# Performance work log

Measured on AMD Instinct MI355X. Metric: run time of the kernel, lower is better.

## Reference

```python
import jax, jax.numpy as jnp
import numpy as np

B, T, C = 4, 2048, 1024
H = 16
D = C // H  # head_dim = 64


def setup_inputs() -> dict:
    key = jax.random.key(0)
    ks = jax.random.split(key, 5)
    scale_in = 1.0 / np.sqrt(C)
    x = jax.random.normal(ks[0], (B, T, C), dtype=jnp.float32)
    w_qkv = jax.random.normal(ks[1], (C, 3 * C), dtype=jnp.float32) * scale_in
    b_qkv = jnp.zeros((3 * C,), dtype=jnp.float32)
    w_proj = jax.random.normal(ks[2], (C, C), dtype=jnp.float32) * scale_in
    b_proj = jnp.zeros((C,), dtype=jnp.float32)
    return {"x": x, "w_qkv": w_qkv, "b_qkv": b_qkv, "w_proj": w_proj, "b_proj": b_proj}


def reference(x, w_qkv, b_qkv, w_proj, b_proj):
    # fused QKV projection: [B,T,3C]
    qkv = x @ w_qkv + b_qkv
    q, k, v = jnp.split(qkv, 3, axis=-1)
    # [B,T,C] -> [B,H,T,D]
    q = q.reshape(B, T, H, D).transpose(0, 2, 1, 3)
    k = k.reshape(B, T, H, D).transpose(0, 2, 1, 3)
    v = v.reshape(B, T, H, D).transpose(0, 2, 1, 3)
    scale = 1.0 / np.sqrt(D)
    scores = jnp.einsum('bhqd,bhkd->bhqk', q, k) * scale  # [B,H,T,T]
    causal = jnp.tril(jnp.ones((T, T), dtype=bool))
    scores = jnp.where(causal, scores, jnp.finfo(scores.dtype).min)
    attn = jax.nn.softmax(scores, axis=-1)
    y = jnp.einsum('bhqk,bhkd->bhqd', attn, v)  # [B,H,T,D]
    y = y.transpose(0, 2, 1, 3).reshape(B, T, C)
    return y @ w_proj + b_proj
```

## Files before the change

### kernel.cpp

```cpp
#include <hip/hip_runtime.h>

typedef unsigned short u16;
typedef unsigned int u32;
typedef unsigned long long u64;
typedef __attribute__((ext_vector_type(8))) short s16x8;
typedef __attribute__((ext_vector_type(4))) float f32x4;

#if __has_builtin(__builtin_amdgcn_exp2f)
#define EXP2(x) __builtin_amdgcn_exp2f(x)
#else
#define EXP2(x) __expf((x) * 0.69314718f)
#endif

#if __has_builtin(__builtin_amdgcn_rcpf)
#define RCP(x) __builtin_amdgcn_rcpf(x)
#else
#define RCP(x) (1.0f / (x))
#endif

#define GLL(gp, lp) __builtin_amdgcn_global_load_lds(                         \
    (const __attribute__((address_space(1))) unsigned int*)(const void*)(gp), \
    (__attribute__((address_space(3))) unsigned int*)(void*)(lp), 16, 0, 0)

__device__ __forceinline__ u16 f2bf(float f) {
    union { float f; u32 u; } v; v.f = f;
    u32 r = v.u + 0x7FFF + ((v.u >> 16) & 1);
    return (u16)(r >> 16);
}

__device__ __forceinline__ u32 pack2_trunc(float a, float b) {
    union { float f; u32 u; } x, y; x.f = a; y.f = b;
    return (x.u >> 16) | (y.u & 0xFFFF0000u);
}

__device__ __forceinline__ float bf2f(u16 b) {
    union { u32 u; float f; } v; v.u = ((u32)b) << 16;
    return v.f;
}

__device__ __forceinline__ s16x8 scale_frag(s16x8 v, float s) {
    s16x8 o;
#pragma unroll
    for (int i = 0; i < 8; i++) o[i] = (short)f2bf(bf2f((u16)v[i]) * s);
    return o;
}

__global__ __launch_bounds__(256) void prep_fused(const float* __restrict__ x,
                                                  u16* __restrict__ x_bf,
                                                  const float* __restrict__ w_qkv,
                                                  u16* __restrict__ wqkvT,
                                                  const float* __restrict__ w_proj,
                                                  u16* __restrict__ wprojT) {
    __shared__ float tile[32][33];
    int bid = blockIdx.x, tid = threadIdx.x;
    if (bid < 8192) {
        size_t i = ((size_t)bid * 256 + tid) * 4;
        float4 f = *(const float4*)(x + i);
        u16 o[4] = { f2bf(f.x), f2bf(f.y), f2bf(f.z), f2bf(f.w) };
        *(u64*)(x_bf + i) =
            (u64)o[0] | ((u64)o[1] << 16) | ((u64)o[2] << 32) | ((u64)o[3] << 48);
        return;
    }
    const float* in;
    u16* out;
    int cols, bx, by;
    if (bid < 8192 + 3072) {
        int l = bid - 8192;
        in = w_qkv; out = wqkvT; cols = 3072; bx = l % 96; by = l / 96;
    } else {
        int l = bid - 11264;
        in = w_proj; out = wprojT; cols = 1024; bx = l & 31; by = l >> 5;
    }
    const int rows = 1024;
    int c0 = bx * 32, r0 = by * 32;
    int tx = tid & 31, ty = tid >> 5;
    for (int i = 0; i < 32; i += 8)
        tile[ty + i][tx] = in[(size_t)(r0 + ty + i) * cols + (c0 + tx)];
    __syncthreads();
    for (int i = 0; i < 32; i += 8)
        out[(size_t)(c0 + ty + i) * rows + (r0 + tx)] = f2bf(tile[tx][ty + i]);
}

template<int MODE, int NB>
__global__ __launch_bounds__(256, 4) void gemm_bt64(const u16* __restrict__ A,
                                                    const u16* __restrict__ BT,
                                                    const float* __restrict__ bias,
                                                    void* __restrict__ O1,
                                                    u16* __restrict__ vT,
                                                    int M, int N, int K) {
    __shared__ u16 SMEM[18432];
    u16* As = SMEM;
    u16* Bs = SMEM + 8192;
    int id = blockIdx.x;
    int xcd = id & 7, s = id >> 3;
    int ni = s % NB, mi8 = s / NB;
    int n0 = ni * 128, m0 = (xcd * 8 + mi8) * 128;
    int tid = threadIdx.x, lane = tid & 63, w = tid >> 6;
    int row16 = lane & 15, quad = lane >> 4;
    int wm = (w >> 1) * 64, wn = (w & 1) * 64;
    f32x4 acc[4][4] = {};

    int lr = lane >> 3;
    int cswz = (lane & 7) ^ lr;
    const u16* Ag = A + (size_t)(m0 + w * 32 + lr) * K + cswz * 8;
    const u16* Bg = BT + (size_t)(n0 + w * 32 + lr) * K + cswz * 8;
    u16* Asl = As + (w * 32) * 64;
    u16* Bsl = Bs + (w * 32) * 64;

    for (int k0 = 0; k0 < K; k0 += 64) {
        __syncthreads();
#pragma unroll
        for (int j = 0; j < 4; j++) {
            GLL(Ag + k0 + (size_t)j * 8 * K, Asl + j * 8 * 64);
            GLL(Bg + k0 + (size_t)j * 8 * K, Bsl + j * 8 * 64);
        }
        __syncthreads();
#pragma unroll
        for (int kk = 0; kk < 2; kk++) {
            s16x8 af[4], bf[4];
#pragma unroll
            for (int mi = 0; mi < 4; mi++)
                af[mi] = *(const s16x8*)&As[(wm + mi * 16 + row16) * 64 +
                                            (((kk * 4 + quad) ^ (row16 & 7)) * 8)];
#pragma unroll
            for (int ni2 = 0; ni2 < 4; ni2++)
                bf[ni2] = *(const s16x8*)&Bs[(wn + ni2 * 16 + row16) * 64 +
                                             (((kk * 4 + quad) ^ (row16 & 7)) * 8)];
#pragma unroll
            for (int mi = 0; mi < 4; mi++)
#pragma unroll
                for (int ni2 = 0; ni2 < 4; ni2++)
                    acc[mi][ni2] = __builtin_amdgcn_mfma_f32_16x16x32_bf16(
                        af[mi], bf[ni2], acc[mi][ni2], 0, 0, 0);
        }
    }

    if (MODE == 0) {
        float* O = (float*)O1;
#pragma unroll
        for (int ni2 = 0; ni2 < 4; ni2++) {
            int col = n0 + wn + ni2 * 16 + row16;
            float bv = bias[col];
#pragma unroll
            for (int mi = 0; mi < 4; mi++)
#pragma unroll
                for (int r = 0; r < 4; r++)
                    O[(size_t)(m0 + wm + mi * 16 + quad * 4 + r) * N + col] =
                        acc[mi][ni2][r] + bv;
        }
    } else if (n0 < 2048) {
        u16* qk = (u16*)O1;
#pragma unroll
        for (int ni2 = 0; ni2 < 4; ni2++) {
            int col = n0 + wn + ni2 * 16 + row16;
            float bv = bias[col];
#pragma unroll
            for (int mi = 0; mi < 4; mi++)
#pragma unroll
                for (int r = 0; r < 4; r++)
                    qk[(size_t)(m0 + wm + mi * 16 + quad * 4 + r) * 2048 + col] =
                        f2bf(acc[mi][ni2][r] + bv);
        }
    } else {
        __syncthreads();
        u16* scr = SMEM + w * 64 * 72;
#pragma unroll
        for (int ni2 = 0; ni2 < 4; ni2++) {
            float bv = bias[n0 + wn + ni2 * 16 + row16];
#pragma unroll
            for (int mi = 0; mi < 4; mi++)
#pragma unroll
                for (int r = 0; r < 4; r++)
                    scr[(ni2 * 16 + row16) * 72 + (mi * 16 + quad * 4 + r)] =
                        f2bf(acc[mi][ni2][r] + bv);
        }
        __syncthreads();
        int r8 = lane >> 3, c8 = lane & 7;
        int vbase = (m0 >> 11) * 1024 + (n0 - 2048) + wn;
        int tb = (m0 & 2047) + wm;
#pragma unroll
        for (int it = 0; it < 8; it++) {
            s16x8 vv = *(const s16x8*)&scr[(it * 8 + r8) * 72 + c8 * 8];
            *(s16x8*)&vT[(size_t)(vbase + it * 8 + r8) * 2048 + tb + c8 * 8] = vv;
        }
    }
}

__global__ __launch_bounds__(256, 2) void attn_kernel(const u16* __restrict__ qk,
                                                      const u16* __restrict__ vT,
                                                      u16* __restrict__ y) {
    __shared__ u16 Kb[2][4096];
    __shared__ u16 Vb[2][4096];
    __shared__ u16 Ps[4][2048];

    int tid = threadIdx.x, lane = tid & 63, w = tid >> 6;
    int row16 = lane & 15, quad = lane >> 4;
    int id = blockIdx.x;
    int xcd = id & 7, slot = id >> 3;
    int qt = 15 - (slot >> 3);
    int bh = ((slot & 7) << 3) | xcd;
    int b = bh >> 4, h = bh & 15;
    const u16* qkb = qk + (size_t)b * 2048 * 2048;
    const u16* vtb = vT + ((size_t)(b * 1024) + h * 64) * 2048;

    int lr = lane >> 3, cswz = (lane & 7) ^ lr;
    const u16* Kg = qkb + (size_t)(w * 16 + lr) * 2048 + 1024 + h * 64 + cswz * 8;
    const u16* Vg = vtb + (size_t)(w * 16 + lr) * 2048 + cswz * 8;
    u16* Psw = Ps[w];
    int sw = row16 & 7;

    s16x8 ones;
#pragma unroll
    for (int i = 0; i < 8; i++) ones[i] = (short)0x3F80;
    const float qs = 0.125f * 1.44269504f;

    int q0 = qt * 128;
    int niter = 2 * qt + 2;
    int qw = q0 + w * 32;

    s16x8 qf[2][2];
#pragma unroll
    for (int mi = 0; mi < 2; mi++) {
        const u16* qp = qkb + (size_t)(qw + mi * 16 + row16) * 2048 + h * 64 + quad * 8;
        qf[mi][0] = scale_frag(*(const s16x8*)qp, qs);
        qf[mi][1] = scale_frag(*(const s16x8*)(qp + 32), qs);
    }

    f32x4 acc_o[2][4] = {};
    f32x4 acc_l[2] = {};

#pragma unroll
    for (int j = 0; j < 2; j++) {
        GLL(Kg + (size_t)j * 8 * 2048, Kb[0] + w * 16 * 64 + j * 8 * 64);
        GLL(Vg + (size_t)j * 8 * 2048, Vb[0] + w * 16 * 64 + j * 8 * 64);
    }

    for (int kb = 0; kb < niter; kb++) {
        int cur = kb & 1;
        __syncthreads();
        if (kb + 1 < niter) {
            int k1 = (kb + 1) * 64;
#pragma unroll
            for (int j = 0; j < 2; j++) {
                GLL(Kg + (size_t)(k1 + j * 8) * 2048, Kb[cur ^ 1] + w * 16 * 64 + j * 8 * 64);
                GLL(Vg + k1 + (size_t)j * 8 * 2048, Vb[cur ^ 1] + w * 16 * 64 + j * 8 * 64);
            }
        }
        int k0 = kb * 64;
        if (k0 > qw + 31) continue;
        const u16* Kc = Kb[cur];
        const u16* Vc = Vb[cur];

        f32x4 sc[2][4];
#pragma unroll
        for (int nk = 0; nk < 4; nk++) {
            s16x8 kf0 = *(const s16x8*)&Kc[(nk * 16 + row16) * 64 + ((quad ^ sw) * 8)];
            s16x8 kf1 = *(const s16x8*)&Kc[(nk * 16 + row16) * 64 + (((4 + quad) ^ sw) * 8)];
#pragma unroll
            for (int mi = 0; mi < 2; mi++) {
                f32x4 z = {};
                z = __builtin_amdgcn_mfma_f32_16x16x32_bf16(kf0, qf[mi][0], z, 0, 0, 0);
                z = __builtin_amdgcn_mfma_f32_16x16x32_bf16(kf1, qf[mi][1], z, 0, 0, 0);
                sc[mi][nk] = z;
            }
        }
        if (k0 + 63 > qw) {
#pragma unroll
            for (int mi = 0; mi < 2; mi++) {
                int qg = qw + mi * 16 + row16;
#pragma unroll
                for (int nk = 0; nk < 4; nk++) {
                    int kbase = k0 + nk * 16 + quad * 4;
#pragma unroll
                    for (int r = 0; r < 4; r++)
                        if (kbase + r > qg) sc[mi][nk][r] = -__builtin_inff();
                }
            }
        }
#pragma unroll
        for (int mi = 0; mi < 2; mi++)
#pragma unroll
            for (int nk = 0; nk < 4; nk++) {
                float p0 = EXP2(sc[mi][nk][0]);
                float p1 = EXP2(sc[mi][nk][1]);
                float p2 = EXP2(sc[mi][nk][2]);
                float p3 = EXP2(sc[mi][nk][3]);
                u32 w0 = pack2_trunc(p0, p1);
                u32 w1 = pack2_trunc(p2, p3);
                int u = nk * 2 + (quad >> 1);
                int eo = ((u ^ sw) * 8) + (quad & 1) * 4;
                *(u64*)&Psw[mi * 1024 + row16 * 64 + eo] = (u64)w0 | ((u64)w1 << 32);
            }
#pragma unroll
        for (int kk = 0; kk < 2; kk++) {
            int co = ((kk * 4 + quad) ^ sw) * 8;
            s16x8 pf0 = *(const s16x8*)&Psw[row16 * 64 + co];
            s16x8 pf1 = *(const s16x8*)&Psw[1024 + row16 * 64 + co];
#pragma unroll
            for (int nd = 0; nd < 4; nd++) {
                s16x8 vf = *(const s16x8*)&Vc[(nd * 16 + row16) * 64 + co];
                acc_o[0][nd] = __builtin_amdgcn_mfma_f32_16x16x32_bf16(pf0, vf, acc_o[0][nd], 0, 0, 0);
                acc_o[1][nd] = __builtin_amdgcn_mfma_f32_16x16x32_bf16(pf1, vf, acc_o[1][nd], 0, 0, 0);
            }
            acc_l[0] = __builtin_amdgcn_mfma_f32_16x16x32_bf16(pf0, ones, acc_l[0], 0, 0, 0);
            acc_l[1] = __builtin_amdgcn_mfma_f32_16x16x32_bf16(pf1, ones, acc_l[1], 0, 0, 0);
        }
    }

#pragma unroll
    for (int mi = 0; mi < 2; mi++) {
        int t0 = qw + mi * 16 + quad * 4;
#pragma unroll
        for (int r = 0; r < 4; r++) {
            float inv = RCP(acc_l[mi][r]);
#pragma unroll
            for (int nd = 0; nd < 4; nd++)
                y[((size_t)b * 2048 + t0 + r) * 1024 + h * 64 + nd * 16 + row16] =
                    f2bf(acc_o[mi][nd][r] * inv);
        }
    }
}

extern "C" void kernel_launch(void* const* d_in, const int* in_sizes, int n_in,
                              void* d_out, int out_size, void* d_ws, size_t ws_size,
                              hipStream_t stream) {
    const float* x      = (const float*)d_in[0];
    const float* w_qkv  = (const float*)d_in[1];
    const float* b_qkv  = (const float*)d_in[2];
    const float* w_proj = (const float*)d_in[3];
    const float* b_proj = (const float*)d_in[4];
    float* out = (float*)d_out;

    u16* ws     = (u16*)d_ws;
    u16* x_bf   = ws;
    u16* wqkvT  = x_bf  + (size_t)8192 * 1024;
    u16* wprojT = wqkvT + (size_t)3072 * 1024;
    u16* qkbuf  = wprojT + (size_t)1024 * 1024;
    u16* vT     = qkbuf + (size_t)8192 * 2048;
    u16* ybf    = vT    + (size_t)4096 * 2048;

    prep_fused<<<dim3(12288), dim3(256), 0, stream>>>(x, x_bf, w_qkv, wqkvT, w_proj, wprojT);
    gemm_bt64<1, 24><<<dim3(1536), 256, 0, stream>>>(x_bf, wqkvT, b_qkv, (void*)qkbuf, vT, 8192, 3072, 1024);
    attn_kernel<<<dim3(1024), 256, 0, stream>>>(qkbuf, vT, ybf);
    gemm_bt64<0, 8><<<dim3(512), 256, 0, stream>>>(ybf, wprojT, b_proj, (void*)out, nullptr, 8192, 1024, 1024);
}
```

Measured before the change: 223.3 us.

## Replace QKV GEMM with 256x128-tile, 512-thread double-buffered kernel

Adds a dedicated QKV projection kernel that uses 256x128 output tiles with 8 waves and BK=64. Global-to-LDS loads are double-buffered and use an XOR-swizzled layout, and MFMA sections run at raised priority. The larger tile raises A/B reuse per block and halves the block count. The trade-off is 96KB of LDS per block and one block per CU, which lowers occupancy and the ability to hide latency.

```diff
diff --git a/kernel.cpp b/kernel.cpp
--- a/kernel.cpp
+++ b/kernel.cpp
@@ -79,6 +79,125 @@
     __syncthreads();
     for (int i = 0; i < 32; i += 8)
         out[(size_t)(c0 + ty + i) * rows + (r0 + tx)] = f2bf(tile[tx][ty + i]);
+}
+
+__global__ __launch_bounds__(512, 1) void gemm_qkv_p2(const u16* __restrict__ A,
+                                                      const u16* __restrict__ BT,
+                                                      const float* __restrict__ bias,
+                                                      u16* __restrict__ qk,
+                                                      u16* __restrict__ vT) {
+    constexpr int K = 1024;
+    __shared__ u16 SM[49152];
+    u16* As = SM;
+    u16* Bs = SM + 32768;
+
+    int id = blockIdx.x;
+    int xcd = id & 7, j = id >> 3;
+    int m0 = (xcd * 4 + j / 24) * 256;
+    int n0 = (j % 24) * 128;
+
+    int tid = threadIdx.x, lane = tid & 63, w = tid >> 6;
+    int row16 = lane & 15, quad = lane >> 4;
+    int wm = w >> 1, wn = w & 1;
+    int swz = row16 & 7;
+
+    int tr = tid >> 3, tc = (tid & 7) ^ (tr & 7);
+    const u16* Ag = A + (size_t)(m0 + tr) * K + tc * 8;
+    const u16* Bg = BT + (size_t)(n0 + tr) * K + tc * 8;
+
+    int aBase = (wm * 64 + row16) * 64;
+    int bBase = (wn * 64 + row16) * 64;
+
+    f32x4 acc[4][4] = {};
+
+#define STGALL(KO, BD) do {                                                    \
+    _Pragma("unroll") for (int q = 0; q < 4; q++)                              \
+        GLL(Ag + (size_t)(q * 64) * K + (KO), As + (BD) * 16384 + q * 4096 + tid * 8); \
+    _Pragma("unroll") for (int u2 = 0; u2 < 2; u2++)                           \
+        GLL(Bg + (size_t)(u2 * 64) * K + (KO), Bs + (BD) * 8192 + u2 * 4096 + tid * 8); \
+} while (0)
+#define BAR __builtin_amdgcn_s_barrier()
+#define WAITL do {                                                             \
+    asm volatile("s_waitcnt lgkmcnt(0)" ::: "memory");                         \
+    __builtin_amdgcn_sched_barrier(0);                                         \
+} while (0)
+#define RD(KKv) do {                                                           \
+    int cx = (((KKv) * 4 + quad) ^ swz) * 8;                                   \
+    _Pragma("unroll") for (int m4 = 0; m4 < 4; m4++)                           \
+        afr[m4] = *(const s16x8*)&As[bufo + aBase + m4 * 16 * 64 + cx];        \
+    _Pragma("unroll") for (int nf = 0; nf < 4; nf++)                           \
+        bfr[nf] = *(const s16x8*)&Bs[bufo2 + bBase + nf * 16 * 64 + cx];       \
+} while (0)
+#define MM do {                                                                \
+    __builtin_amdgcn_s_setprio(1);                                             \
+    _Pragma("unroll") for (int m4 = 0; m4 < 4; m4++)                           \
+        _Pragma("unroll") for (int nf = 0; nf < 4; nf++)                       \
+            acc[m4][nf] = __builtin_amdgcn_mfma_f32_16x16x32_bf16(             \
+                afr[m4], bfr[nf], acc[m4][nf], 0, 0, 0);                       \
+    __builtin_amdgcn_s_setprio(0);                                             \
+} while (0)
+
+    STGALL(0, 0);
+    STGALL(64, 1);
+    asm volatile("s_waitcnt vmcnt(6)" ::: "memory");
+    BAR;
+
+    for (int t = 0; t < 16; ++t) {
+        int buf = t & 1;
+        int bufo = buf * 16384, bufo2 = buf * 8192;
+        s16x8 afr[4], bfr[4];
+        RD(0);
+        BAR; WAITL; MM; BAR;
+        RD(1);
+        BAR; WAITL; MM; BAR;
+        if (t < 14) {
+            STGALL((size_t)(t + 2) * 64, buf);
+            asm volatile("s_waitcnt vmcnt(6)" ::: "memory");
+        } else if (t == 14) {
+            asm volatile("s_waitcnt vmcnt(0)" ::: "memory");
+        }
+        BAR;
+    }
+#undef STGALL
+#undef RD
+#undef MM
+#undef WAITL
+
+    if (n0 < 2048) {
+#pragma unroll
+        for (int nf = 0; nf < 4; nf++) {
+            int col = n0 + wn * 64 + nf * 16 + row16;
+            float bv = bias[col];
+#pragma unroll
+            for (int m4 = 0; m4 < 4; m4++)
+#pragma unroll
+                for (int r = 0; r < 4; r++)
+                    qk[(size_t)(m0 + wm * 64 + m4 * 16 + quad * 4 + r) * 2048 + col] =
+                        f2bf(acc[m4][nf][r] + bv);
+        }
+    } else {
+        u16* scr = SM + w * 4608;
+        __syncthreads();
+#pragma unroll
+        for (int nf = 0; nf < 4; nf++) {
+            float bv = bias[n0 + wn * 64 + nf * 16 + row16];
+#pragma unroll
+            for (int m4 = 0; m4 < 4; m4++)
+#pragma unroll
+                for (int r = 0; r < 4; r++)
+                    scr[(nf * 16 + row16) * 72 + (m4 * 16 + quad * 4 + r)] =
+                        f2bf(acc[m4][nf][r] + bv);
+        }
+        __syncthreads();
+        int r8 = lane >> 3, c8l = lane & 7;
+        int vbase = (m0 >> 11) * 1024 + (n0 - 2048) + wn * 64;
+        int tb = (m0 & 2047) + wm * 64;
+#pragma unroll
+        for (int it = 0; it < 8; it++) {
+            s16x8 vv = *(const s16x8*)&scr[(it * 8 + r8) * 72 + c8l * 8];
+            *(s16x8*)&vT[(size_t)(vbase + it * 8 + r8) * 2048 + tb + c8l * 8] = vv;
+        }
+    }
 }
 
 template<int MODE, int NB>
@@ -340,7 +459,7 @@
     u16* ybf    = vT    + (size_t)4096 * 2048;
 
     prep_fused<<<dim3(12288), dim3(256), 0, stream>>>(x, x_bf, w_qkv, wqkvT, w_proj, wprojT);
-    gemm_bt64<1, 24><<<dim3(1536), 256, 0, stream>>>(x_bf, wqkvT, b_qkv, (void*)qkbuf, vT, 8192, 3072, 1024);
+    gemm_qkv_p2<<<dim3(768), dim3(512), 0, stream>>>(x_bf, wqkvT, b_qkv, qkbuf, vT);
     attn_kernel<<<dim3(1024), 256, 0, stream>>>(qkbuf, vT, ybf);
     gemm_bt64<0, 8><<<dim3(512), 256, 0, stream>>>(ybf, wprojT, b_proj, (void*)out, nullptr, 8192, 1024, 1024);
 }
```

Result: slower. 228.1 us (+2.2%).
